# Kernel tuning notes

Hardware: AMD Instinct MI355X
Metric: run time of the kernel (lower is better)

## Reference

```python
import jax, jax.numpy as jnp
import numpy as np

K = 512          # num_embeddings
D = 8            # latent_dim
DECAY = 0.99     # ema_decay
EPS = 1e-5


def setup_inputs() -> dict:
    key = jax.random.key(0)
    k1, k2 = jax.random.split(key)
    z = jax.random.normal(k1, (64, D, 64, 64), dtype=jnp.float32)
    # codebook initialized uniform(-1/K, 1/K) as in the torch module
    codebook = jax.random.uniform(k2, (K, D), dtype=jnp.float32,
                                  minval=-1.0 / K, maxval=1.0 / K)
    ema_cluster_size = jnp.zeros((K,), dtype=jnp.float32)
    ema_w = jnp.zeros((K, D), dtype=jnp.float32)
    return {"z": z, "codebook": codebook,
            "ema_cluster_size": ema_cluster_size, "ema_w": ema_w}


def reference(z, codebook, ema_cluster_size, ema_w):
    B, C, H, W = z.shape
    # (B, HW, C) flattened latents, matching z.view(B,C,-1).permute(0,2,1)
    flat = z.reshape(B, C, H * W).transpose(0, 2, 1)

    # cdist p=2: ||z||^2 - 2 z.e + ||e||^2, then sqrt (argmin unaffected,
    # but we keep the sqrt for faithfulness to torch.cdist)
    z_sq = jnp.sum(flat * flat, axis=-1, keepdims=True)        # (B, N, 1)
    e_sq = jnp.sum(codebook * codebook, axis=-1)               # (K,)
    dots = jnp.einsum('bnd,kd->bnk', flat, codebook)           # (B, N, K)
    distances = jnp.sqrt(jnp.maximum(z_sq - 2.0 * dots + e_sq, 0.0))

    indices = jnp.argmin(distances, axis=-1)                   # (B, N) int

    # embedding gather with the OLD codebook (as in the torch forward)
    z_q = codebook[indices]                                    # (B, N, D)
    z_q = z_q.transpose(0, 2, 1).reshape(B, C, H, W)

    commitment_loss = jnp.mean((jax.lax.stop_gradient(z_q) - z) ** 2)
    loss = commitment_loss  # use_ema=True branch

    # ---- EMA in-place codebook update (buffers) ----
    idx_flat = indices.reshape(-1)                             # (B*N,)
    inp_flat = flat.reshape(-1, C)                             # (B*N, D)
    counts = jax.ops.segment_sum(jnp.ones_like(idx_flat, dtype=z.dtype),
                                 idx_flat, num_segments=K)     # (K,)
    sums = jax.ops.segment_sum(inp_flat, idx_flat, num_segments=K)  # (K, D)

    new_cs = ema_cluster_size * DECAY + counts * (1.0 - DECAY)
    new_w = ema_w * DECAY + sums * (1.0 - DECAY)
    n = jnp.sum(new_cs)
    cs_smoothed = (new_cs + EPS) / (n + K * EPS) * n
    new_codebook = new_w / cs_smoothed[:, None]

    return z_q, loss, new_codebook, cs_smoothed, new_w
```

## Files before the change

### kernel.cpp

```cpp
#include <hip/hip_runtime.h>

constexpr int Kc   = 512;
constexpr int Dc   = 8;
constexpr int HWc  = 4096;
constexpr int CHWc = Dc * HWc;
constexpr int Mc   = 64 * HWc;
constexpr int TOTALc = Mc * Dc;

constexpr int REP      = 8;
constexpr int RSTRIDE  = 4616;
constexpr int ACC_FLOATS = REP * RSTRIDE;

__global__ __launch_bounds__(256) void vq_prep(const float* __restrict__ cb,
                                               float* __restrict__ ws) {
    const int tid = blockIdx.x * 256 + threadIdx.x;
    float4* w4 = (float4*)ws;
    for (int i = tid; i < ACC_FLOATS / 4; i += gridDim.x * 256)
        w4[i] = float4{0.f, 0.f, 0.f, 0.f};
    if (blockIdx.x == 0) {
        for (int k = threadIdx.x; k < Kc; k += 256) {
            float s = 0.f;
#pragma unroll
            for (int c = 0; c < Dc; ++c) {
                const float e = cb[k * Dc + c];
                s = fmaf(e, e, s);
            }
            ws[ACC_FLOATS + k] = s;
        }
    }
}

__global__ __launch_bounds__(512, 8) void vq_main(const float* __restrict__ z,
                                                  const float* __restrict__ cb,
                                                  const float* __restrict__ esq,
                                                  float* __restrict__ ws,
                                                  float* __restrict__ zq) {
    __shared__ float s_counts[Kc];
    __shared__ float s_sums[Kc * Dc];
    __shared__ float s_mn[4][256];
    __shared__ int   s_im[4][256];
    __shared__ float s_loss;

    const int t = threadIdx.x;
    for (int i = t; i < Kc; i += 512) s_counts[i] = 0.f;
    for (int i = t; i < Kc * Dc; i += 512) s_sums[i] = 0.f;
    if (t == 0) s_loss = 0.f;

    const int vl = t & 127;
    const int g  = __builtin_amdgcn_readfirstlane(t >> 7);
    const int k0 = g << 7;

    const int base = blockIdx.x * 256;
    const int n0 = (base + vl) & (HWc - 1);
    const int b  = base >> 12;
    const float* zb = z + b * CHWc + n0;

    float zz0[Dc], zz1[Dc];
#pragma unroll
    for (int c = 0; c < Dc; ++c) {
        zz0[c] = -2.0f * zb[c * HWc];
        zz1[c] = -2.0f * zb[c * HWc + 128];
    }

    float mn0 = 3.4e38f, mn1 = 3.4e38f;
    int   i0 = k0, i1 = k0;
#pragma unroll 4
    for (int kk = 0; kk < 128; ++kk) {
        const int k = k0 + kk;
        float a0 = esq[k];
        float a1 = a0;
#pragma unroll
        for (int c = 0; c < Dc; ++c) {
            const float e = cb[k * Dc + c];
            a0 = fmaf(zz0[c], e, a0);
            a1 = fmaf(zz1[c], e, a1);
        }
        const bool c0 = a0 < mn0;
        mn0 = c0 ? a0 : mn0;
        i0  = c0 ? k  : i0;
        const bool c1 = a1 < mn1;
        mn1 = c1 ? a1 : mn1;
        i1  = c1 ? k  : i1;
    }
    s_mn[g][vl]       = mn0;
    s_im[g][vl]       = i0;
    s_mn[g][vl + 128] = mn1;
    s_im[g][vl + 128] = i1;
    __syncthreads();

    if (t < 256) {
        const int v = t;
        float mn = s_mn[0][v];
        int   im = s_im[0][v];
#pragma unroll
        for (int gg = 1; gg < 4; ++gg) {
            const float m2 = s_mn[gg][v];
            const int   j2 = s_im[gg][v];
            const bool  c2 = m2 < mn;
            mn = c2 ? m2 : mn;
            im = c2 ? j2 : im;
        }

        const float4* cb4 = (const float4*)cb;
        const float4 qa = cb4[im * 2], qb = cb4[im * 2 + 1];
        const float q[Dc] = {qa.x, qa.y, qa.z, qa.w, qb.x, qb.y, qb.z, qb.w};

        const int nv = (base + v) & (HWc - 1);
        const float* zv = z + b * CHWc + nv;
        float* zqv = zq + b * CHWc + nv;
        float lsum = 0.f;
        float zr[Dc];
#pragma unroll
        for (int c = 0; c < Dc; ++c) {
            zr[c] = zv[c * HWc];
            zqv[c * HWc] = q[c];
            const float d = q[c] - zr[c];
            lsum = fmaf(d, d, lsum);
        }

        unsafeAtomicAdd(&s_counts[im], 1.0f);
#pragma unroll
        for (int c = 0; c < Dc; ++c)
            unsafeAtomicAdd(&s_sums[im * Dc + c], zr[c]);
        unsafeAtomicAdd(&s_loss, lsum);
    }
    __syncthreads();

    float* acc = ws + (blockIdx.x & (REP - 1)) * RSTRIDE;
    for (int i = t; i < Kc; i += 512) {
        const float val = s_counts[i];
        if (val != 0.f) unsafeAtomicAdd(&acc[i], val);
    }
    for (int i = t; i < Kc * Dc; i += 512) {
        const float val = s_sums[i];
        if (val != 0.f) unsafeAtomicAdd(&acc[512 + i], val);
    }
    if (t == 0) unsafeAtomicAdd(&acc[4608], s_loss);
}

__global__ __launch_bounds__(512) void vq_final(const float* __restrict__ ws,
                                                const float* __restrict__ ema_cs,
                                                const float* __restrict__ ema_w,
                                                float* __restrict__ out) {
    constexpr float DEC  = 0.99f;
    constexpr float OMD  = (float)(1.0 - 0.99);
    constexpr float EPSf = 1e-5f;
    constexpr float KEPS = (float)(512 * 1e-5);
    __shared__ float red[512];
    __shared__ float s_cs[512];

    const int t = threadIdx.x;
    float cnt = 0.f;
#pragma unroll
    for (int r = 0; r < REP; ++r) cnt += ws[r * RSTRIDE + t];
    const float ncs = ema_cs[t] * DEC + cnt * OMD;
    red[t] = ncs;
    __syncthreads();
    for (int s = 256; s > 0; s >>= 1) {
        if (t < s) red[t] += red[t + s];
        __syncthreads();
    }
    const float n  = red[0];
    const float cs = (ncs + EPSf) / (n + KEPS) * n;
    s_cs[t] = cs;

    float* out_loss = out + TOTALc;
    float* out_cb   = out + TOTALc + 1;
    float* out_cs   = out_cb + Kc * Dc;
    float* out_nw   = out_cs + Kc;

    out_cs[t] = cs;
    __syncthreads();

    for (int e = t; e < Kc * Dc; e += 512) {
        float sm = 0.f;
#pragma unroll
        for (int r = 0; r < REP; ++r) sm += ws[r * RSTRIDE + 512 + e];
        const float nw = ema_w[e] * DEC + sm * OMD;
        out_nw[e] = nw;
        out_cb[e] = nw / s_cs[e >> 3];
    }
    if (t == 0) {
        float ls = 0.f;
#pragma unroll
        for (int r = 0; r < REP; ++r) ls += ws[r * RSTRIDE + 4608];
        out_loss[0] = ls * (1.0f / 2097152.0f);
    }
}

extern "C" void kernel_launch(void* const* d_in, const int* in_sizes, int n_in,
                              void* d_out, int out_size, void* d_ws, size_t ws_size,
                              hipStream_t stream) {
    const float* z      = (const float*)d_in[0];
    const float* cb     = (const float*)d_in[1];
    const float* ema_cs = (const float*)d_in[2];
    const float* ema_w  = (const float*)d_in[3];
    float* out = (float*)d_out;
    float* ws  = (float*)d_ws;

    vq_prep<<<32, 256, 0, stream>>>(cb, ws);
    vq_main<<<Mc / 256, 512, 0, stream>>>(z, cb, ws + ACC_FLOATS, ws, out);
    vq_final<<<1, 512, 0, stream>>>(ws, ema_cs, ema_w, out);
}
```

Measured before the change: 113.1 us.

## Vectorize codebook loads, reuse cached z, and parallelize final EMA kernel

Result: slower. 161.0 us (+42.4%).

```diff
diff --git a/kernel.cpp b/kernel.cpp
--- a/kernel.cpp
+++ b/kernel.cpp
@@ -35,10 +35,10 @@
                                                   const float* __restrict__ esq,
                                                   float* __restrict__ ws,
                                                   float* __restrict__ zq) {
+    __shared__ float s_mn[4][256];
+    __shared__ int   s_im[4][256];
     __shared__ float s_counts[Kc];
     __shared__ float s_sums[Kc * Dc];
-    __shared__ float s_mn[4][256];
-    __shared__ int   s_im[4][256];
     __shared__ float s_loss;
 
     const int t = threadIdx.x;
@@ -62,19 +62,30 @@
         zz1[c] = -2.0f * zb[c * HWc + 128];
     }
 
+    unsigned long long cbp = (unsigned long long)cb;
+    unsigned long long eqp = (unsigned long long)esq;
+    asm("" : "+v"(cbp));
+    asm("" : "+v"(eqp));
+    const float4* cb4v = (const float4*)cbp;
+    const float*  esqv = (const float*)eqp;
+
     float mn0 = 3.4e38f, mn1 = 3.4e38f;
     int   i0 = k0, i1 = k0;
-#pragma unroll 4
+#pragma unroll 2
     for (int kk = 0; kk < 128; ++kk) {
         const int k = k0 + kk;
-        float a0 = esq[k];
-        float a1 = a0;
-#pragma unroll
-        for (int c = 0; c < Dc; ++c) {
-            const float e = cb[k * Dc + c];
-            a0 = fmaf(zz0[c], e, a0);
-            a1 = fmaf(zz1[c], e, a1);
-        }
+        const float4 e0 = cb4v[k * 2];
+        const float4 e1 = cb4v[k * 2 + 1];
+        const float  ev = esqv[k];
+        float a0 = fmaf(zz0[0], e0.x, ev);
+        float a1 = fmaf(zz1[0], e0.x, ev);
+        a0 = fmaf(zz0[1], e0.y, a0);  a1 = fmaf(zz1[1], e0.y, a1);
+        a0 = fmaf(zz0[2], e0.z, a0);  a1 = fmaf(zz1[2], e0.z, a1);
+        a0 = fmaf(zz0[3], e0.w, a0);  a1 = fmaf(zz1[3], e0.w, a1);
+        a0 = fmaf(zz0[4], e1.x, a0);  a1 = fmaf(zz1[4], e1.x, a1);
+        a0 = fmaf(zz0[5], e1.y, a0);  a1 = fmaf(zz1[5], e1.y, a1);
+        a0 = fmaf(zz0[6], e1.z, a0);  a1 = fmaf(zz1[6], e1.z, a1);
+        a0 = fmaf(zz0[7], e1.w, a0);  a1 = fmaf(zz1[7], e1.w, a1);
         const bool c0 = a0 < mn0;
         mn0 = c0 ? a0 : mn0;
         i0  = c0 ? k  : i0;
@@ -105,14 +116,16 @@
         const float4 qa = cb4[im * 2], qb = cb4[im * 2 + 1];
         const float q[Dc] = {qa.x, qa.y, qa.z, qa.w, qb.x, qb.y, qb.z, qb.w};
 
-        const int nv = (base + v) & (HWc - 1);
-        const float* zv = z + b * CHWc + nv;
+        float zr[Dc];
+#pragma unroll
+        for (int c = 0; c < Dc; ++c)
+            zr[c] = -0.5f * ((t < 128) ? zz0[c] : zz1[c]);
+
+        const int nv = (base & (HWc - 1)) + v;
         float* zqv = zq + b * CHWc + nv;
         float lsum = 0.f;
-        float zr[Dc];
 #pragma unroll
         for (int c = 0; c < Dc; ++c) {
-            zr[c] = zv[c * HWc];
             zqv[c * HWc] = q[c];
             const float d = q[c] - zr[c];
             lsum = fmaf(d, d, lsum);
@@ -169,22 +182,25 @@
     float* out_cs   = out_cb + Kc * Dc;
     float* out_nw   = out_cs + Kc;
 
-    out_cs[t] = cs;
-    __syncthreads();
-
-    for (int e = t; e < Kc * Dc; e += 512) {
+    __syncthreads();
+
+    const int blk = blockIdx.x;
+    if (blk == 0) {
+        out_cs[t] = cs;
+        if (t == 0) {
+            float ls = 0.f;
+#pragma unroll
+            for (int r = 0; r < REP; ++r) ls += ws[r * RSTRIDE + 4608];
+            out_loss[0] = ls * (1.0f / 2097152.0f);
+        }
+    } else {
+        const int e = (blk - 1) * 512 + t;
         float sm = 0.f;
 #pragma unroll
         for (int r = 0; r < REP; ++r) sm += ws[r * RSTRIDE + 512 + e];
         const float nw = ema_w[e] * DEC + sm * OMD;
         out_nw[e] = nw;
         out_cb[e] = nw / s_cs[e >> 3];
-    }
-    if (t == 0) {
-        float ls = 0.f;
-#pragma unroll
-        for (int r = 0; r < REP; ++r) ls += ws[r * RSTRIDE + 4608];
-        out_loss[0] = ls * (1.0f / 2097152.0f);
     }
 }
 
@@ -200,5 +216,5 @@
 
     vq_prep<<<32, 256, 0, stream>>>(cb, ws);
     vq_main<<<Mc / 256, 512, 0, stream>>>(z, cb, ws + ACC_FLOATS, ws, out);
-    vq_final<<<1, 512, 0, stream>>>(ws, ema_cs, ema_w, out);
-}
+    vq_final<<<9, 512, 0, stream>>>(ws, ema_cs, ema_w, out);
+}
```
